# Performance work log

Hardware: AMD Instinct MI355X
Metric: run time of the kernel (lower is better)

The kernel has to match this reference:

```python
import jax, jax.numpy as jnp
import numpy as np

C = 64            # in_channels
IC = C // 2       # inter_channels (channel_rate=2)
R = 16            # reduction_ratio
EPS = 1e-5


def setup_inputs() -> dict:
    key = jax.random.key(0)
    ks = jax.random.split(key, 16)
    s = 0.05
    return {
        "x": jax.random.normal(ks[0], (16, C, 64, 25), dtype=jnp.float32),
        # 1x1 conv projections (common_v, key, query): [out, in] + bias
        "Wv": jax.random.normal(ks[1], (IC, C), dtype=jnp.float32) * s,
        "bv": jax.random.normal(ks[2], (IC,), dtype=jnp.float32) * s,
        "Wk": jax.random.normal(ks[3], (IC, C), dtype=jnp.float32) * s,
        "bk": jax.random.normal(ks[4], (IC,), dtype=jnp.float32) * s,
        "Wq": jax.random.normal(ks[5], (IC, C), dtype=jnp.float32) * s,
        "bq": jax.random.normal(ks[6], (IC,), dtype=jnp.float32) * s,
        # Trans_s: conv1x1 back to C + BatchNorm2d params (nonzero so output is non-trivial)
        "Wt": jax.random.normal(ks[7], (C, IC), dtype=jnp.float32) * s,
        "bt": jax.random.normal(ks[8], (C,), dtype=jnp.float32) * s,
        "gamma": jax.random.normal(ks[9], (C,), dtype=jnp.float32) * 0.5 + 1.0,
        "beta": jax.random.normal(ks[10], (C,), dtype=jnp.float32) * s,
        # ChannelGate MLP: Linear(C, C//R), Linear(C//R, C)
        "W1": jax.random.normal(ks[11], (C // R, C), dtype=jnp.float32) * s,
        "b1": jax.random.normal(ks[12], (C // R,), dtype=jnp.float32) * s,
        "W2": jax.random.normal(ks[13], (C, C // R), dtype=jnp.float32) * s,
        "b2": jax.random.normal(ks[14], (C,), dtype=jnp.float32) * s,
    }


def _conv1x1(x, W, b):
    # x: [N, Cin, T, V]; W: [Cout, Cin]
    return jnp.einsum('nctv,oc->notv', x, W) + b[None, :, None, None]


def reference(x, Wv, bv, Wk, bk, Wq, bq, Wt, bt, gamma, beta, W1, b1, W2, b2):
    N, Cc, T, V = x.shape
    TV = T * V
    ic = Wv.shape[0]

    v_x = _conv1x1(x, Wv, bv).reshape(N, ic, TV).transpose(0, 2, 1)  # [N, TV, ic]
    k_x = _conv1x1(x, Wk, bk).reshape(N, ic, TV).transpose(0, 2, 1)  # [N, TV, ic]
    q_x = _conv1x1(x, Wq, bq).reshape(N, ic, TV)                      # [N, ic, TV]

    # Unscaled dot-product attention over TV tokens (full [N, TV, TV] matrix)
    A = jnp.einsum('nti,nis->nts', k_x, q_x)
    attn = jax.nn.softmax(A, axis=-1)
    p = jnp.einsum('nts,nsi->nti', attn, v_x)                         # [N, TV, ic]
    p = p.transpose(0, 2, 1).reshape(N, ic, T, V)

    # Trans_s: conv1x1 + BatchNorm2d (training-mode batch statistics)
    p = _conv1x1(p, Wt, bt)
    mean = p.mean(axis=(0, 2, 3), keepdims=True)
    var = p.var(axis=(0, 2, 3), keepdims=True)
    p = (p - mean) * jax.lax.rsqrt(var + EPS)
    p = p * gamma[None, :, None, None] + beta[None, :, None, None]

    # ChannelGate (avg pool only) applied to original x
    avg = x.mean(axis=(2, 3))                                          # [N, C]
    h = jax.nn.relu(avg @ W1.T + b1)
    gate = jax.nn.sigmoid(h @ W2.T + b2)                               # [N, C]

    return gate[:, :, None, None] * p + x
```

## Files before the change

### kernel.cpp

```cpp
#include <hip/hip_runtime.h>
#include <hip/hip_bf16.h>
#include <math.h>

#define NB   16
#define CC   64
#define ICH  32
#define TV   1600
#define NTV  (NB*TV)

typedef __bf16 bf16x8 __attribute__((ext_vector_type(8)));
typedef float  f32x4  __attribute__((ext_vector_type(4)));

__global__ __launch_bounds__(256) void proj_gate_kernel(
    const float* __restrict__ x,
    const float* __restrict__ Wv, const float* __restrict__ bv,
    const float* __restrict__ Wk, const float* __restrict__ bk,
    const float* __restrict__ Wq, const float* __restrict__ bq,
    __bf16* __restrict__ Qb, __bf16* __restrict__ Kb,
    __bf16* __restrict__ VTb, float* __restrict__ AVG) {
  if (blockIdx.x >= 400) {
    int b = blockIdx.x - 400;
    int n = b >> 2, cq = b & 3;
    int c16 = threadIdx.x >> 4, l = threadIdx.x & 15;
    int c = cq * 16 + c16;
    const float4* xp = (const float4*)(x + ((size_t)n * CC + c) * TV) + l;
    float s = 0.f;
#pragma unroll
    for (int i = 0; i < 25; ++i) {
      float4 v = xp[i * 16];
      s += v.x + v.y + v.z + v.w;
    }
#pragma unroll
    for (int off = 8; off >= 1; off >>= 1) s += __shfl_down(s, off, 16);
    if (l == 0) AVG[n * CC + c] = s * (1.0f / (float)TV);
    return;
  }

  int tile = blockIdx.x >> 2;
  int og   = blockIdx.x & 3;
  int ob = og * 8;
  int tvIdx = tile * 256 + threadIdx.x;
  int n = tvIdx / TV, tv = tvIdx % TV;

  float av[8], ak[8], aq[8];
#pragma unroll
  for (int j = 0; j < 8; ++j) { av[j] = bv[ob+j]; ak[j] = bk[ob+j]; aq[j] = bq[ob+j]; }

  const float* xp = x + (size_t)n * CC * TV + tv;
#pragma unroll 8
  for (int c = 0; c < CC; ++c) {
    float xc = xp[c * TV];
#pragma unroll
    for (int j = 0; j < 8; ++j) {
      av[j] = fmaf(Wv[(ob + j) * CC + c], xc, av[j]);
      ak[j] = fmaf(Wk[(ob + j) * CC + c], xc, ak[j]);
      aq[j] = fmaf(Wq[(ob + j) * CC + c], xc, aq[j]);
    }
  }

  bf16x8 t;
#pragma unroll
  for (int j = 0; j < 8; ++j) t[j] = (__bf16)ak[j];
  int base = (n * TV + tv) * ICH + ob;
  *(bf16x8*)(Qb + base) = t;
#pragma unroll
  for (int j = 0; j < 8; ++j) t[j] = (__bf16)aq[j];
  *(bf16x8*)(Kb + base) = t;
#pragma unroll
  for (int j = 0; j < 8; ++j)
    VTb[(n * ICH + ob + j) * TV + tv] = (__bf16)av[j];
}

__global__ __launch_bounds__(256) void attn_kernel(
    const __bf16* __restrict__ Qb, const __bf16* __restrict__ Kb,
    const __bf16* __restrict__ VTb, float* __restrict__ P) {
  __shared__ float lds[4 * 2 * 16 * 68];
  int b = blockIdx.x;
  int r8 = b & 7, qq = b >> 3;
  int n = r8 * 2 + (qq >= 50 ? 1 : 0);
  int rowTile = (qq >= 50) ? qq - 50 : qq;
  int row0 = rowTile * 32;

  int w = threadIdx.x >> 6;
  int lane = threadIdx.x & 63;
  int m = lane & 15, q = lane >> 4;

  float* Pw0 = lds + w * 2176;
  float* Pw1 = Pw0 + 1088;

  const __bf16* Qn = Qb  + (size_t)n * TV * ICH;
  const __bf16* Kn = Kb  + (size_t)n * TV * ICH;
  const __bf16* Vn = VTb + (size_t)n * ICH * TV;

  bf16x8 aQ0 = *(const bf16x8*)(Qn + (row0 + m) * ICH + q * 8);
  bf16x8 aQ1 = *(const bf16x8*)(Qn + (row0 + 16 + m) * ICH + q * 8);

  f32x4 o00 = {0.f,0.f,0.f,0.f}, o01 = {0.f,0.f,0.f,0.f};
  f32x4 o10 = {0.f,0.f,0.f,0.f}, o11 = {0.f,0.f,0.f,0.f};
  float ls0 = 0.f, ls1 = 0.f;
  const f32x4 zero = {0.f,0.f,0.f,0.f};

  int nch = (w == 3) ? 7 : 6;
  for (int j = 0; j < nch; ++j) {
    int s0 = (4 * j + (3 - w)) * 64;
#pragma unroll
    for (int st = 0; st < 4; ++st) {
      bf16x8 bK = *(const bf16x8*)(Kn + (s0 + st * 16 + m) * ICH + q * 8);
      f32x4 a0 = __builtin_amdgcn_mfma_f32_16x16x32_bf16(aQ0, bK, zero, 0, 0, 0);
      f32x4 a1 = __builtin_amdgcn_mfma_f32_16x16x32_bf16(aQ1, bK, zero, 0, 0, 0);
#pragma unroll
      for (int r = 0; r < 4; ++r) {
        Pw0[(q * 4 + r) * 68 + st * 16 + m] = __expf(a0[r]);
        Pw1[(q * 4 + r) * 68 + st * 16 + m] = __expf(a1[r]);
      }
    }
    asm volatile("s_waitcnt lgkmcnt(0)" ::: "memory");
#pragma unroll
    for (int kc = 0; kc < 2; ++kc) {
      const f32x4* pr0 = (const f32x4*)(Pw0 + m * 68 + kc * 32);
      const f32x4* pr1 = (const f32x4*)(Pw1 + m * 68 + kc * 32);
      f32x4 p0a = pr0[q * 2], p0b = pr0[q * 2 + 1];
      f32x4 p1a = pr1[q * 2], p1b = pr1[q * 2 + 1];
      bf16x8 aP0, aP1;
#pragma unroll
      for (int r = 0; r < 4; ++r) {
        ls0 += p0a[r] + p0b[r];
        ls1 += p1a[r] + p1b[r];
        aP0[r]     = (__bf16)p0a[r];
        aP0[4 + r] = (__bf16)p0b[r];
        aP1[r]     = (__bf16)p1a[r];
        aP1[4 + r] = (__bf16)p1b[r];
      }
#pragma unroll
      for (int ict = 0; ict < 2; ++ict) {
        bf16x8 bV = *(const bf16x8*)(Vn + (ict * 16 + m) * TV + s0 + kc * 32 + q * 8);
        if (ict == 0) {
          o00 = __builtin_amdgcn_mfma_f32_16x16x32_bf16(aP0, bV, o00, 0, 0, 0);
          o10 = __builtin_amdgcn_mfma_f32_16x16x32_bf16(aP1, bV, o10, 0, 0, 0);
        } else {
          o01 = __builtin_amdgcn_mfma_f32_16x16x32_bf16(aP0, bV, o01, 0, 0, 0);
          o11 = __builtin_amdgcn_mfma_f32_16x16x32_bf16(aP1, bV, o11, 0, 0, 0);
        }
      }
    }
  }

  ls0 += __shfl_xor(ls0, 16, 64); ls0 += __shfl_xor(ls0, 32, 64);
  ls1 += __shfl_xor(ls1, 16, 64); ls1 += __shfl_xor(ls1, 32, 64);

  __syncthreads();
  float* mp = lds + (w * 64 + lane) * 18;
#pragma unroll
  for (int r = 0; r < 4; ++r) {
    mp[r]      = o00[r]; mp[4 + r]  = o01[r];
    mp[8 + r]  = o10[r]; mp[12 + r] = o11[r];
  }
  mp[16] = ls0; mp[17] = ls1;
  __syncthreads();
  if (w == 0) {
#pragma unroll
    for (int ww = 1; ww < 4; ++ww) {
      const float* sp = lds + (ww * 64 + lane) * 18;
#pragma unroll
      for (int r = 0; r < 4; ++r) {
        o00[r] += sp[r];      o01[r] += sp[4 + r];
        o10[r] += sp[8 + r];  o11[r] += sp[12 + r];
      }
      ls0 += sp[16]; ls1 += sp[17];
    }
#pragma unroll
    for (int r = 0; r < 4; ++r) {
      float lr0 = __shfl(ls0, q * 4 + r, 64);
      float lr1 = __shfl(ls1, q * 4 + r, 64);
      float i0 = 1.f / lr0, i1 = 1.f / lr1;
      int pb0 = (n * TV + row0 + q * 4 + r) * ICH;
      int pb1 = pb0 + 16 * ICH;
      P[pb0 + m]      = o00[r] * i0;
      P[pb0 + 16 + m] = o01[r] * i0;
      P[pb1 + m]      = o10[r] * i1;
      P[pb1 + 16 + m] = o11[r] * i1;
    }
  }
}

__global__ __launch_bounds__(256) void stats_kernel(
    const float* __restrict__ P, const float* __restrict__ Wt,
    const float* __restrict__ bt, float* __restrict__ PS2) {
  int cg = blockIdx.x / 100;
  int tb = blockIdx.x % 100;
  int tvIdx = tb * 256 + threadIdx.x;
  int n = tvIdx / TV, tv = tvIdx % TV;

  union { f32x4 v[8]; float f[32]; } p;
  const f32x4* pp = (const f32x4*)(P + ((size_t)(n * TV + tv)) * ICH);
#pragma unroll
  for (int u = 0; u < 8; ++u) p.v[u] = pp[u];

  __shared__ float red[2][4][8];
  int w = threadIdx.x >> 6, lane = threadIdx.x & 63;
#pragma unroll
  for (int j = 0; j < 8; ++j) {
    int c = cg * 8 + j;
    float y = bt[c];
#pragma unroll
    for (int i = 0; i < ICH; ++i) y = fmaf(Wt[c * ICH + i], p.f[i], y);
    float y2 = y * y;
#pragma unroll
    for (int off = 32; off >= 1; off >>= 1) {
      y  += __shfl_xor(y,  off, 64);
      y2 += __shfl_xor(y2, off, 64);
    }
    if (lane == 0) { red[0][w][j] = y; red[1][w][j] = y2; }
  }
  __syncthreads();
  if (threadIdx.x < 16) {
    int which = threadIdx.x >> 3, j = threadIdx.x & 7;
    float s = red[which][0][j] + red[which][1][j] +
              red[which][2][j] + red[which][3][j];
    PS2[blockIdx.x * 16 + which * 8 + j] = s;
  }
}

__global__ __launch_bounds__(128) void finalize_stats(
    const float* __restrict__ PS2, const float* __restrict__ gamma,
    const float* __restrict__ beta, const float* __restrict__ AVG,
    const float* __restrict__ W1, const float* __restrict__ b1,
    const float* __restrict__ W2, const float* __restrict__ b2,
    float* __restrict__ SS, float* __restrict__ GATE) {
  int t = threadIdx.x;
  __shared__ float sh[NB][4];
  if (t < 64) {
    int c = t, cg = c >> 3, j = c & 7;
    float s = 0.f, ss = 0.f;
    for (int b = 0; b < 100; ++b) {
      int base = (cg * 100 + b) * 16;
      s  += PS2[base + j];
      ss += PS2[base + 8 + j];
    }
    float mean = s * (1.f / (float)NTV);
    float var  = ss * (1.f / (float)NTV) - mean * mean;
    float scale = rsqrtf(var + 1e-5f) * gamma[c];
    SS[c] = scale;
    SS[64 + c] = beta[c] - mean * scale;
    int n = t >> 2, jj = t & 3;
    float h = b1[jj];
    for (int c2 = 0; c2 < CC; ++c2)
      h = fmaf(W1[jj * CC + c2], AVG[n * CC + c2], h);
    sh[n][jj] = fmaxf(h, 0.f);
  }
  __syncthreads();
#pragma unroll
  for (int u = 0; u < 8; ++u) {
    int idx = t * 8 + u;
    int n = idx >> 6, c = idx & 63;
    float g = b2[c];
#pragma unroll
    for (int jj = 0; jj < 4; ++jj) g = fmaf(W2[c * 4 + jj], sh[n][jj], g);
    GATE[idx] = 1.f / (1.f + __expf(-g));
  }
}

__global__ __launch_bounds__(256) void apply_kernel(
    const float* __restrict__ P, const float* __restrict__ Wt,
    const float* __restrict__ bt, const float* __restrict__ SS,
    const float* __restrict__ gate, const float* __restrict__ x,
    float* __restrict__ out) {
  int cg = blockIdx.x / 100;
  int tb = blockIdx.x % 100;
  int tvIdx = tb * 256 + threadIdx.x;
  int n = tvIdx / TV, tv = tvIdx % TV;

  union { f32x4 v[8]; float f[32]; } p;
  const f32x4* pp = (const f32x4*)(P + ((size_t)(n * TV + tv)) * ICH);
#pragma unroll
  for (int u = 0; u < 8; ++u) p.v[u] = pp[u];

#pragma unroll
  for (int j = 0; j < 8; ++j) {
    int c = cg * 8 + j;
    float y = bt[c];
#pragma unroll
    for (int i = 0; i < ICH; ++i) y = fmaf(Wt[c * ICH + i], p.f[i], y);
    size_t idx = ((size_t)(n * CC + c)) * TV + tv;
    out[idx] = gate[n * CC + c] * fmaf(y, SS[c], SS[64 + c]) + x[idx];
  }
}

extern "C" void kernel_launch(void* const* d_in, const int* in_sizes, int n_in,
                              void* d_out, int out_size, void* d_ws, size_t ws_size,
                              hipStream_t stream) {
  const float* x     = (const float*)d_in[0];
  const float* Wv    = (const float*)d_in[1];
  const float* bv    = (const float*)d_in[2];
  const float* Wk    = (const float*)d_in[3];
  const float* bk    = (const float*)d_in[4];
  const float* Wq    = (const float*)d_in[5];
  const float* bq    = (const float*)d_in[6];
  const float* Wt    = (const float*)d_in[7];
  const float* bt    = (const float*)d_in[8];
  const float* gamma = (const float*)d_in[9];
  const float* beta  = (const float*)d_in[10];
  const float* W1    = (const float*)d_in[11];
  const float* b1    = (const float*)d_in[12];
  const float* W2    = (const float*)d_in[13];
  const float* b2    = (const float*)d_in[14];
  float* out = (float*)d_out;
  char* ws = (char*)d_ws;

  const size_t E = 819200;
  __bf16* Qb  = (__bf16*)(ws);
  __bf16* Kb  = (__bf16*)(ws + 2*E);
  __bf16* VTb = (__bf16*)(ws + 4*E);
  float*  P   = (float*) (ws + 6*E);
  float*  PS2 = (float*) (ws + 10*E);
  float*  SS  = (float*) (ws + 10*E + 51200);
  float*  GATE= (float*) (ws + 10*E + 51712);
  float*  AVG = out;

  proj_gate_kernel<<<464, 256, 0, stream>>>(x, Wv, bv, Wk, bk, Wq, bq,
                                            Qb, Kb, VTb, AVG);
  attn_kernel<<<NB * 50, 256, 0, stream>>>(Qb, Kb, VTb, P);
  stats_kernel<<<800, 256, 0, stream>>>(P, Wt, bt, PS2);
  finalize_stats<<<1, 128, 0, stream>>>(PS2, gamma, beta, AVG,
                                        W1, b1, W2, b2, SS, GATE);
  apply_kernel<<<800, 256, 0, stream>>>(P, Wt, bt, SS, GATE, x, out);
}
```

Before: 158.6 us.

## Store attention probabilities as bf16 in LDS and process two key chunks per iteration

The attention kernel now converts exp scores to bf16 before writing them to LDS, halving LDS traffic and letting the PV MFMA operand load straight from LDS without per-element conversion. Row sums are accumulated in registers right after the exp, in the MFMA output layout, and reduced with xor shuffles at the end. The loop is unrolled to handle two 64-key chunks per iteration, which gives more independent MFMA and load work between LDS waits. The cost is more registers and a larger per-wave LDS region, and rounding to bf16 happens before the probabilities are staged rather than after they are read back.

```diff
diff --git a/kernel.cpp b/kernel.cpp
--- a/kernel.cpp
+++ b/kernel.cpp
@@ -74,7 +74,7 @@
 __global__ __launch_bounds__(256) void attn_kernel(
     const __bf16* __restrict__ Qb, const __bf16* __restrict__ Kb,
     const __bf16* __restrict__ VTb, float* __restrict__ P) {
-  __shared__ float lds[4 * 2 * 16 * 68];
+  __shared__ __bf16 lds[4 * 4608];
   int b = blockIdx.x;
   int r8 = b & 7, qq = b >> 3;
   int n = r8 * 2 + (qq >= 50 ? 1 : 0);
@@ -85,8 +85,7 @@
   int lane = threadIdx.x & 63;
   int m = lane & 15, q = lane >> 4;
 
-  float* Pw0 = lds + w * 2176;
-  float* Pw1 = Pw0 + 1088;
+  __bf16* Pw = lds + w * 4608;
 
   const __bf16* Qn = Qb  + (size_t)n * TV * ICH;
   const __bf16* Kn = Kb  + (size_t)n * TV * ICH;
@@ -97,43 +96,52 @@
 
   f32x4 o00 = {0.f,0.f,0.f,0.f}, o01 = {0.f,0.f,0.f,0.f};
   f32x4 o10 = {0.f,0.f,0.f,0.f}, o11 = {0.f,0.f,0.f,0.f};
-  float ls0 = 0.f, ls1 = 0.f;
+  f32x4 ls0 = {0.f,0.f,0.f,0.f}, ls1 = {0.f,0.f,0.f,0.f};
   const f32x4 zero = {0.f,0.f,0.f,0.f};
 
   int nch = (w == 3) ? 7 : 6;
-  for (int j = 0; j < nch; ++j) {
-    int s0 = (4 * j + (3 - w)) * 64;
+
+  for (int jj = 0; jj < nch; jj += 2) {
+    int sA = (4 * jj + (3 - w)) * 64;
+    bool hasB = (jj + 1) < nch;
+    int sB = hasB ? (4 * (jj + 1) + (3 - w)) * 64 : sA;
+
 #pragma unroll
     for (int st = 0; st < 4; ++st) {
-      bf16x8 bK = *(const bf16x8*)(Kn + (s0 + st * 16 + m) * ICH + q * 8);
+      bf16x8 bK = *(const bf16x8*)(Kn + (sA + st * 16 + m) * ICH + q * 8);
       f32x4 a0 = __builtin_amdgcn_mfma_f32_16x16x32_bf16(aQ0, bK, zero, 0, 0, 0);
       f32x4 a1 = __builtin_amdgcn_mfma_f32_16x16x32_bf16(aQ1, bK, zero, 0, 0, 0);
 #pragma unroll
       for (int r = 0; r < 4; ++r) {
-        Pw0[(q * 4 + r) * 68 + st * 16 + m] = __expf(a0[r]);
-        Pw1[(q * 4 + r) * 68 + st * 16 + m] = __expf(a1[r]);
+        float e0 = __expf(a0[r]); ls0[r] += e0;
+        float e1 = __expf(a1[r]); ls1[r] += e1;
+        Pw[(q * 4 + r) * 72 + st * 16 + m]        = (__bf16)e0;
+        Pw[1152 + (q * 4 + r) * 72 + st * 16 + m] = (__bf16)e1;
+      }
+    }
+    if (hasB) {
+#pragma unroll
+      for (int st = 0; st < 4; ++st) {
+        bf16x8 bK = *(const bf16x8*)(Kn + (sB + st * 16 + m) * ICH + q * 8);
+        f32x4 a0 = __builtin_amdgcn_mfma_f32_16x16x32_bf16(aQ0, bK, zero, 0, 0, 0);
+        f32x4 a1 = __builtin_amdgcn_mfma_f32_16x16x32_bf16(aQ1, bK, zero, 0, 0, 0);
+#pragma unroll
+        for (int r = 0; r < 4; ++r) {
+          float e0 = __expf(a0[r]); ls0[r] += e0;
+          float e1 = __expf(a1[r]); ls1[r] += e1;
+          Pw[2304 + (q * 4 + r) * 72 + st * 16 + m] = (__bf16)e0;
+          Pw[3456 + (q * 4 + r) * 72 + st * 16 + m] = (__bf16)e1;
+        }
       }
     }
     asm volatile("s_waitcnt lgkmcnt(0)" ::: "memory");
 #pragma unroll
     for (int kc = 0; kc < 2; ++kc) {
-      const f32x4* pr0 = (const f32x4*)(Pw0 + m * 68 + kc * 32);
-      const f32x4* pr1 = (const f32x4*)(Pw1 + m * 68 + kc * 32);
-      f32x4 p0a = pr0[q * 2], p0b = pr0[q * 2 + 1];
-      f32x4 p1a = pr1[q * 2], p1b = pr1[q * 2 + 1];
-      bf16x8 aP0, aP1;
-#pragma unroll
-      for (int r = 0; r < 4; ++r) {
-        ls0 += p0a[r] + p0b[r];
-        ls1 += p1a[r] + p1b[r];
-        aP0[r]     = (__bf16)p0a[r];
-        aP0[4 + r] = (__bf16)p0b[r];
-        aP1[r]     = (__bf16)p1a[r];
-        aP1[4 + r] = (__bf16)p1b[r];
-      }
+      bf16x8 aP0 = *(const bf16x8*)(Pw + m * 72 + kc * 32 + q * 8);
+      bf16x8 aP1 = *(const bf16x8*)(Pw + 1152 + m * 72 + kc * 32 + q * 8);
 #pragma unroll
       for (int ict = 0; ict < 2; ++ict) {
-        bf16x8 bV = *(const bf16x8*)(Vn + (ict * 16 + m) * TV + s0 + kc * 32 + q * 8);
+        bf16x8 bV = *(const bf16x8*)(Vn + (ict * 16 + m) * TV + sA + kc * 32 + q * 8);
         if (ict == 0) {
           o00 = __builtin_amdgcn_mfma_f32_16x16x32_bf16(aP0, bV, o00, 0, 0, 0);
           o10 = __builtin_amdgcn_mfma_f32_16x16x32_bf16(aP1, bV, o10, 0, 0, 0);
@@ -143,36 +151,59 @@
         }
       }
     }
-  }
-
-  ls0 += __shfl_xor(ls0, 16, 64); ls0 += __shfl_xor(ls0, 32, 64);
-  ls1 += __shfl_xor(ls1, 16, 64); ls1 += __shfl_xor(ls1, 32, 64);
+    if (hasB) {
+#pragma unroll
+      for (int kc = 0; kc < 2; ++kc) {
+        bf16x8 aP0 = *(const bf16x8*)(Pw + 2304 + m * 72 + kc * 32 + q * 8);
+        bf16x8 aP1 = *(const bf16x8*)(Pw + 3456 + m * 72 + kc * 32 + q * 8);
+#pragma unroll
+        for (int ict = 0; ict < 2; ++ict) {
+          bf16x8 bV = *(const bf16x8*)(Vn + (ict * 16 + m) * TV + sB + kc * 32 + q * 8);
+          if (ict == 0) {
+            o00 = __builtin_amdgcn_mfma_f32_16x16x32_bf16(aP0, bV, o00, 0, 0, 0);
+            o10 = __builtin_amdgcn_mfma_f32_16x16x32_bf16(aP1, bV, o10, 0, 0, 0);
+          } else {
+            o01 = __builtin_amdgcn_mfma_f32_16x16x32_bf16(aP0, bV, o01, 0, 0, 0);
+            o11 = __builtin_amdgcn_mfma_f32_16x16x32_bf16(aP1, bV, o11, 0, 0, 0);
+          }
+        }
+      }
+    }
+  }
+
+#pragma unroll
+  for (int mask = 1; mask <= 8; mask <<= 1) {
+#pragma unroll
+    for (int r = 0; r < 4; ++r) {
+      ls0[r] += __shfl_xor(ls0[r], mask, 64);
+      ls1[r] += __shfl_xor(ls1[r], mask, 64);
+    }
+  }
 
   __syncthreads();
-  float* mp = lds + (w * 64 + lane) * 18;
+  float* mf = (float*)lds;
+  float* mp = mf + (w * 64 + lane) * 24;
 #pragma unroll
   for (int r = 0; r < 4; ++r) {
     mp[r]      = o00[r]; mp[4 + r]  = o01[r];
     mp[8 + r]  = o10[r]; mp[12 + r] = o11[r];
-  }
-  mp[16] = ls0; mp[17] = ls1;
+    mp[16 + r] = ls0[r]; mp[20 + r] = ls1[r];
+  }
   __syncthreads();
   if (w == 0) {
 #pragma unroll
     for (int ww = 1; ww < 4; ++ww) {
-      const float* sp = lds + (ww * 64 + lane) * 18;
+      const float* sp = mf + (ww * 64 + lane) * 24;
 #pragma unroll
       for (int r = 0; r < 4; ++r) {
         o00[r] += sp[r];      o01[r] += sp[4 + r];
         o10[r] += sp[8 + r];  o11[r] += sp[12 + r];
-      }
-      ls0 += sp[16]; ls1 += sp[17];
+        ls0[r] += sp[16 + r]; ls1[r] += sp[20 + r];
+      }
     }
 #pragma unroll
     for (int r = 0; r < 4; ++r) {
-      float lr0 = __shfl(ls0, q * 4 + r, 64);
-      float lr1 = __shfl(ls1, q * 4 + r, 64);
-      float i0 = 1.f / lr0, i1 = 1.f / lr1;
+      float i0 = 1.f / ls0[r], i1 = 1.f / ls1[r];
       int pb0 = (n * TV + row0 + q * 4 + r) * ICH;
       int pb1 = pb0 + 16 * ICH;
       P[pb0 + m]      = o00[r] * i0;
```

Result: no change. 157.4 us (-0.8%).
